# Kernel tuning notes

Hardware: AMD Instinct MI355X
Metric: run time of the kernel (lower is better)

## Reference

```python
import jax, jax.numpy as jnp
import numpy as np

N_NODES = 20000
N_EDGES = 200000
D_IN, D_H1, D_H2, D_OUT = 1433, 1000, 500, 7


def setup_inputs() -> dict:
    key = jax.random.key(0)
    ks = jax.random.split(key, 8)
    features = jax.random.normal(ks[0], (N_NODES, D_IN), dtype=jnp.float32)
    src = jax.random.randint(ks[1], (N_EDGES,), 0, N_NODES)
    dst = jax.random.randint(ks[2], (N_EDGES,), 0, N_NODES)
    W1 = jax.random.normal(ks[3], (D_IN, D_H1), dtype=jnp.float32) * 0.02
    b1 = jnp.zeros((D_H1,), dtype=jnp.float32)
    W2 = jax.random.normal(ks[4], (D_H1, D_H2), dtype=jnp.float32) * 0.02
    b2 = jnp.zeros((D_H2,), dtype=jnp.float32)
    W3 = jax.random.normal(ks[5], (D_H2, D_OUT), dtype=jnp.float32) * 0.02
    b3 = jnp.zeros((D_OUT,), dtype=jnp.float32)
    return {"features": features, "src": src, "dst": dst,
            "W1": W1, "b1": b1, "W2": W2, "b2": b2, "W3": W3, "b3": b3}


def reference(features, src, dst, W1, b1, W2, b2, W3, b3):
    N = features.shape[0]

    def agg(x):  # sum_tensors over incoming neighbors: h_i = sum_{(j->i) in E} x_j
        return jax.ops.segment_sum(x[src], dst, num_segments=N)

    # GCN layer 1: aggregate -> linear -> relu
    x = jax.nn.relu(agg(features) @ W1 + b1)       # [N, 1000]
    # GCN layer 2: aggregate -> linear -> relu (dropout = identity in eval)
    x = jax.nn.relu(agg(x) @ W2 + b2)              # [N, 500]
    # output linear -> relu (dropout = identity in eval)
    x = jax.nn.relu(x @ W3 + b3)                   # [N, 7]
    return x
```

## Files before the change

kernel.cpp:

```cpp
#include <hip/hip_runtime.h>
#include <hip/hip_bf16.h>


#define N_NODES 20000
#define N_EDGES 200000
#define D_IN    1433
#define D_H1    1000
#define D_H2    500
#define D_OUT   7

#define MPAD    20096
#define K1PAD   1440
#define N1PAD   1024
#define K2PAD   1024
#define N2PAD   512
#define H1STR   1008
#define H2STR   504
#define MBLK    157

typedef __attribute__((ext_vector_type(8))) short short8;
typedef __attribute__((ext_vector_type(8))) unsigned short ushort8_t;
typedef __attribute__((ext_vector_type(4))) float f32x4;

__device__ __forceinline__ unsigned short bf16_rne(float x) {
    unsigned int u = __float_as_uint(x);
    u = (u + 0x7FFFu + ((u >> 16) & 1u)) >> 16;
    return (unsigned short)u;
}
__device__ __forceinline__ float bf16_up(unsigned short h) {
    return __uint_as_float((unsigned int)h << 16);
}

__device__ __forceinline__ void gl_lds16(const unsigned short* g, unsigned short* lds) {
    __builtin_amdgcn_global_load_lds(
        (const __attribute__((address_space(1))) unsigned int*)g,
        (__attribute__((address_space(3))) unsigned int*)lds, 16, 0, 0);
}

__global__ __launch_bounds__(256) void count_deg(const int* __restrict__ dst,
                                                 int* __restrict__ offs) {
    int e = blockIdx.x * 256 + threadIdx.x;
    if (e < N_EDGES) atomicAdd(&offs[dst[e] + 1], 1);
}

__global__ __launch_bounds__(1024) void scan_csr(int* __restrict__ offs,
                                                 int* __restrict__ cursor, int n) {
    __shared__ int wsum[16];
    __shared__ int s_carry;
    const int t = threadIdx.x, lane = t & 63, wv = t >> 6;
    if (t == 0) s_carry = 0;
    __syncthreads();
    for (int base = 0; base < n; base += 1024) {
        int i = base + t;
        int v = (i < n) ? offs[i] : 0;
        #pragma unroll
        for (int s = 1; s < 64; s <<= 1) {
            int u = __shfl_up(v, s, 64);
            if (lane >= s) v += u;
        }
        if (lane == 63) wsum[wv] = v;
        __syncthreads();
        int prefix = s_carry;
        for (int k = 0; k < wv; ++k) prefix += wsum[k];
        v += prefix;
        if (i < n) {
            offs[i] = v;
            if (i < N_NODES) cursor[i] = v;
        }
        __syncthreads();
        if (t == 1023) s_carry = v;
    }
}

__global__ __launch_bounds__(256) void fill_csr(const int* __restrict__ src,
                                                const int* __restrict__ dst,
                                                int* __restrict__ cursor,
                                                int* __restrict__ srcs) {
    int e = blockIdx.x * 256 + threadIdx.x;
    if (e < N_EDGES) {
        int pos = atomicAdd(&cursor[dst[e]], 1);
        srcs[pos] = src[e];
    }
}

__global__ __launch_bounds__(256) void cast_features(const float* __restrict__ F,
                                                     unsigned int* __restrict__ out) {
    int row = blockIdx.x;
    int t = threadIdx.x;
    const float* fr = F + (size_t)row * D_IN;
    bool live = row < N_NODES;
    for (int kk = t; kk < K1PAD / 2; kk += 256) {
        int k0 = kk * 2;
        float a = (live && k0     < D_IN) ? fr[k0]     : 0.f;
        float b = (live && k0 + 1 < D_IN) ? fr[k0 + 1] : 0.f;
        out[(size_t)row * (K1PAD / 2) + kk] =
            (unsigned int)bf16_rne(a) | ((unsigned int)bf16_rne(b) << 16);
    }
}

template <int SR, int SC, int DR, int DC>
__global__ __launch_bounds__(256) void transpose_cast_pad(const float* __restrict__ src,
                                                          unsigned short* __restrict__ dst) {
    __shared__ float tile[32][33];
    int c0 = blockIdx.x * 32;
    int r0 = blockIdx.y * 32;
    int tx = threadIdx.x & 31, ty = threadIdx.x >> 5;
    #pragma unroll
    for (int p = 0; p < 4; ++p) {
        int r = r0 + ty + p * 8, c = c0 + tx;
        tile[ty + p * 8][tx] = (r < SR && c < SC) ? src[(size_t)r * SC + c] : 0.f;
    }
    __syncthreads();
    #pragma unroll
    for (int p = 0; p < 4; ++p) {
        int dr = c0 + ty + p * 8;
        int dc = r0 + tx;
        if (dr < DR && dc < DC) dst[(size_t)dr * DC + dc] = bf16_rne(tile[tx][ty + p * 8]);
    }
}

template <int KPAD, int NB>
__global__ __launch_bounds__(256) void gemm_mfma(const unsigned short* __restrict__ A,
                                                 const unsigned short* __restrict__ B,
                                                 unsigned short* __restrict__ C,
                                                 int M, int N, int OSTR) {
    __shared__ __align__(16) unsigned short sA[128 * 32];
    __shared__ __align__(16) unsigned short sB[128 * 32];
    const int bid = blockIdx.x;
    const int xcd = bid & 7;
    const int tt  = bid >> 3;
    const int nb  = tt % NB;
    const int mb  = (tt / NB) * 8 + xcd;
    if (mb >= MBLK) return;

    const int t = threadIdx.x;
    const int w = t >> 6, lane = t & 63;
    const int m0 = mb * 128, n0 = nb * 128;
    const int wm = (w >> 1) * 64, wn = (w & 1) * 64;

    const int srow = lane >> 2;
    const int skc  = ((lane & 3) ^ ((lane >> 3) & 3)) * 8;
    const int mrow = lane & 15, quad = lane >> 4;
    const int rslot = ((quad ^ ((mrow >> 1) & 3)) & 3) * 8;

    const unsigned short* Aptr = A + (size_t)(m0 + srow) * KPAD + skc;
    const unsigned short* Bptr = B + (size_t)(n0 + srow) * KPAD + skc;

    f32x4 acc[4][4] = {};

    for (int k0 = 0; k0 < KPAD; k0 += 32) {
        #pragma unroll
        for (int c = 0; c < 2; ++c) {
            int rbase = c * 64 + w * 16;
            gl_lds16(Aptr + (size_t)rbase * KPAD, &sA[rbase * 32]);
            gl_lds16(Bptr + (size_t)rbase * KPAD, &sB[rbase * 32]);
        }
        Aptr += 32; Bptr += 32;
        __syncthreads();

        short8 af[4], bf[4];
        #pragma unroll
        for (int mt = 0; mt < 4; ++mt)
            af[mt] = *(const short8*)&sA[(wm + mt * 16 + mrow) * 32 + rslot];
        #pragma unroll
        for (int nt = 0; nt < 4; ++nt)
            bf[nt] = *(const short8*)&sB[(wn + nt * 16 + mrow) * 32 + rslot];
        #pragma unroll
        for (int mt = 0; mt < 4; ++mt)
            #pragma unroll
            for (int nt = 0; nt < 4; ++nt)
                acc[mt][nt] = __builtin_amdgcn_mfma_f32_16x16x32_bf16(
                    af[mt], bf[nt], acc[mt][nt], 0, 0, 0);
        __syncthreads();
    }

    #pragma unroll
    for (int mt = 0; mt < 4; ++mt) {
        int m = m0 + wm + mt * 16 + quad * 4;
        #pragma unroll
        for (int nt = 0; nt < 4; ++nt) {
            int n = n0 + wn + nt * 16 + mrow;
            if (n >= N) continue;
            #pragma unroll
            for (int r = 0; r < 4; ++r)
                if (m + r < M) C[(size_t)(m + r) * OSTR + n] = bf16_rne(acc[mt][nt][r]);
        }
    }
}

__global__ __launch_bounds__(128) void agg1_bf16(const unsigned short* __restrict__ H,
                                                 const int* __restrict__ offs,
                                                 const int* __restrict__ srcs,
                                                 const float* __restrict__ bias,
                                                 unsigned short* __restrict__ X) {
    const int i = blockIdx.x, t = threadIdx.x;
    const bool active = t < 125;
    const int tc = active ? t : 124;
    ushort8_t o = (ushort8_t)0;
    if (i < N_NODES) {
        const int beg = offs[i], end = offs[i + 1];
        float s[8] = {};
        for (int e = beg; e < end; ++e) {
            const int j = srcs[e];
            ushort8_t v = *(const ushort8_t*)(H + (size_t)j * H1STR + tc * 8);
            #pragma unroll
            for (int u = 0; u < 8; ++u) s[u] += bf16_up(v[u]);
        }
        if (active) {
            #pragma unroll
            for (int u = 0; u < 8; ++u)
                o[u] = bf16_rne(fmaxf(s[u] + bias[t * 8 + u], 0.f));
        }
    }
    *(ushort8_t*)(X + (size_t)i * K2PAD + t * 8) = o;
}

__global__ __launch_bounds__(128) void agg2_out(const unsigned short* __restrict__ H,
                                                const int* __restrict__ offs,
                                                const int* __restrict__ srcs,
                                                const float* __restrict__ b2,
                                                const float* __restrict__ W3,
                                                const float* __restrict__ b3,
                                                float* __restrict__ out) {
    __shared__ float red[2][8];
    const int i = blockIdx.x, t = threadIdx.x;
    const bool active = t < 125;
    const int tc = active ? t : 124;
    const int beg = offs[i], end = offs[i + 1];
    float s[4] = {};
    for (int e = beg; e < end; ++e) {
        const int j = srcs[e];
        ushort4 v = *(const ushort4*)(H + (size_t)j * H2STR + tc * 4);
        s[0] += bf16_up(v.x); s[1] += bf16_up(v.y);
        s[2] += bf16_up(v.z); s[3] += bf16_up(v.w);
    }
    float acc[D_OUT] = {};
    if (active) {
        #pragma unroll
        for (int u = 0; u < 4; ++u) {
            float x = fmaxf(s[u] + b2[t * 4 + u], 0.f);
            const float* wr = W3 + (size_t)(t * 4 + u) * D_OUT;
            #pragma unroll
            for (int j = 0; j < D_OUT; ++j) acc[j] += x * wr[j];
        }
    }
    #pragma unroll
    for (int j = 0; j < D_OUT; ++j)
        #pragma unroll
        for (int off = 32; off; off >>= 1) acc[j] += __shfl_down(acc[j], off);
    const int lane = t & 63, wave = t >> 6;
    if (lane == 0) {
        #pragma unroll
        for (int j = 0; j < D_OUT; ++j) red[wave][j] = acc[j];
    }
    __syncthreads();
    if (t == 0) {
        #pragma unroll
        for (int j = 0; j < D_OUT; ++j)
            out[(size_t)i * D_OUT + j] = fmaxf(red[0][j] + red[1][j] + b3[j], 0.f);
    }
}

extern "C" void kernel_launch(void* const* d_in, const int* in_sizes, int n_in,
                              void* d_out, int out_size, void* d_ws, size_t ws_size,
                              hipStream_t stream) {
    const float* features = (const float*)d_in[0];
    const int*   src      = (const int*)d_in[1];
    const int*   dst      = (const int*)d_in[2];
    const float* W1       = (const float*)d_in[3];
    const float* b1       = (const float*)d_in[4];
    const float* W2       = (const float*)d_in[5];
    const float* b2       = (const float*)d_in[6];
    const float* W3       = (const float*)d_in[7];
    const float* b3       = (const float*)d_in[8];
    float* out = (float*)d_out;

    char* ws = (char*)d_ws;
    unsigned short* Fbf  = (unsigned short*)(ws + 0);
    unsigned short* X1bf = (unsigned short*)(ws + 0);
    unsigned short* H1   = (unsigned short*)(ws + 57876480);
    unsigned short* H2   = (unsigned short*)(ws + 57876480);
    unsigned short* W1T  = (unsigned short*)(ws + 98196480);
    unsigned short* W2T  = (unsigned short*)(ws + 101145600);
    int* offs   = (int*)(ws + 102194176);
    int* cursor = (int*)(ws + 102274304);
    int* srcs   = (int*)(ws + 102354432);

    hipMemsetAsync(offs, 0, (N_NODES + 1) * sizeof(int), stream);
    count_deg<<<(N_EDGES + 255) / 256, 256, 0, stream>>>(dst, offs);
    scan_csr<<<1, 1024, 0, stream>>>(offs, cursor, N_NODES + 1);
    fill_csr<<<(N_EDGES + 255) / 256, 256, 0, stream>>>(src, dst, cursor, srcs);

    cast_features<<<MPAD, 256, 0, stream>>>(features, (unsigned int*)Fbf);
    transpose_cast_pad<D_IN, D_H1, N1PAD, K1PAD>
        <<<dim3(N1PAD / 32, K1PAD / 32), 256, 0, stream>>>(W1, W1T);
    transpose_cast_pad<D_H1, D_H2, N2PAD, K2PAD>
        <<<dim3(N2PAD / 32, K2PAD / 32), 256, 0, stream>>>(W2, W2T);

    gemm_mfma<K1PAD, N1PAD / 128><<<8 * (N1PAD / 128) * 20, 256, 0, stream>>>(
        Fbf, W1T, H1, N_NODES, D_H1, H1STR);
    agg1_bf16<<<MPAD, 128, 0, stream>>>(H1, offs, srcs, b1, X1bf);

    gemm_mfma<K2PAD, N2PAD / 128><<<8 * (N2PAD / 128) * 20, 256, 0, stream>>>(
        X1bf, W2T, H2, N_NODES, D_H2, H2STR);
    agg2_out<<<N_NODES, 128, 0, stream>>>(H2, offs, srcs, b2, W3, b3, out);
}
```

Baseline: 457.5 us.

## Double GEMM K-tile to 64 with new LDS swizzle; unroll gather loops by four

The MFMA GEMM now stages 64-wide K slices into shared memory, using a new XOR swizzle, and runs two MFMA sub-steps per slice. This halves the number of barrier pairs per K loop. K1 is padded to 1472 so it divides by 64, and workspace offsets are shifted to match. Both aggregation kernels unroll the neighbor gather by four to keep more independent loads in flight. The larger padding adds a small amount of wasted work, and the doubled LDS footprint may lower occupancy.

New measurement: 439.3 us. 4.0% less time.

```diff
diff --git a/kernel.cpp b/kernel.cpp
--- a/kernel.cpp
+++ b/kernel.cpp
@@ -10,7 +10,7 @@
 #define D_OUT   7
 
 #define MPAD    20096
-#define K1PAD   1440
+#define K1PAD   1472
 #define N1PAD   1024
 #define K2PAD   1024
 #define N2PAD   512
@@ -124,8 +124,8 @@
                                                  const unsigned short* __restrict__ B,
                                                  unsigned short* __restrict__ C,
                                                  int M, int N, int OSTR) {
-    __shared__ __align__(16) unsigned short sA[128 * 32];
-    __shared__ __align__(16) unsigned short sB[128 * 32];
+    __shared__ __align__(16) unsigned short sA[128 * 64];
+    __shared__ __align__(16) unsigned short sB[128 * 64];
     const int bid = blockIdx.x;
     const int xcd = bid & 7;
     const int tt  = bid >> 3;
@@ -138,39 +138,45 @@
     const int m0 = mb * 128, n0 = nb * 128;
     const int wm = (w >> 1) * 64, wn = (w & 1) * 64;
 
-    const int srow = lane >> 2;
-    const int skc  = ((lane & 3) ^ ((lane >> 3) & 3)) * 8;
+    const int srowo = lane >> 3;
+    const int skc   = ((lane & 7) ^ srowo) * 8;
     const int mrow = lane & 15, quad = lane >> 4;
-    const int rslot = ((quad ^ ((mrow >> 1) & 3)) & 3) * 8;
-
-    const unsigned short* Aptr = A + (size_t)(m0 + srow) * KPAD + skc;
-    const unsigned short* Bptr = B + (size_t)(n0 + srow) * KPAD + skc;
+
+    const unsigned short* Aptr = A + (size_t)(m0 + srowo) * KPAD + skc;
+    const unsigned short* Bptr = B + (size_t)(n0 + srowo) * KPAD + skc;
 
     f32x4 acc[4][4] = {};
 
-    for (int k0 = 0; k0 < KPAD; k0 += 32) {
-        #pragma unroll
-        for (int c = 0; c < 2; ++c) {
-            int rbase = c * 64 + w * 16;
-            gl_lds16(Aptr + (size_t)rbase * KPAD, &sA[rbase * 32]);
-            gl_lds16(Bptr + (size_t)rbase * KPAD, &sB[rbase * 32]);
-        }
-        Aptr += 32; Bptr += 32;
+    for (int k0 = 0; k0 < KPAD; k0 += 64) {
+        #pragma unroll
+        for (int c = 0; c < 4; ++c) {
+            const int rbase = c * 32 + w * 8;
+            gl_lds16(Aptr + (size_t)rbase * KPAD, &sA[rbase * 64]);
+            gl_lds16(Bptr + (size_t)rbase * KPAD, &sB[rbase * 64]);
+        }
+        Aptr += 64; Bptr += 64;
         __syncthreads();
 
-        short8 af[4], bf[4];
-        #pragma unroll
-        for (int mt = 0; mt < 4; ++mt)
-            af[mt] = *(const short8*)&sA[(wm + mt * 16 + mrow) * 32 + rslot];
-        #pragma unroll
-        for (int nt = 0; nt < 4; ++nt)
-            bf[nt] = *(const short8*)&sB[(wn + nt * 16 + mrow) * 32 + rslot];
-        #pragma unroll
-        for (int mt = 0; mt < 4; ++mt)
-            #pragma unroll
-            for (int nt = 0; nt < 4; ++nt)
-                acc[mt][nt] = __builtin_amdgcn_mfma_f32_16x16x32_bf16(
-                    af[mt], bf[nt], acc[mt][nt], 0, 0, 0);
+        #pragma unroll
+        for (int s = 0; s < 2; ++s) {
+            short8 af[4], bf[4];
+            #pragma unroll
+            for (int mt = 0; mt < 4; ++mt) {
+                int r = wm + mt * 16 + mrow;
+                af[mt] = *(const short8*)&sA[r * 64 + (((s * 4 + quad) ^ (mrow & 7)) * 8)];
+            }
+            #pragma unroll
+            for (int nt = 0; nt < 4; ++nt) {
+                int r = wn + nt * 16 + mrow;
+                bf[nt] = *(const short8*)&sB[r * 64 + (((s * 4 + quad) ^ (mrow & 7)) * 8)];
+            }
+            #pragma unroll
+            for (int mt = 0; mt < 4; ++mt)
+                #pragma unroll
+                for (int nt = 0; nt < 4; ++nt)
+                    acc[mt][nt] = __builtin_amdgcn_mfma_f32_16x16x32_bf16(
+                        af[mt], bf[nt], acc[mt][nt], 0, 0, 0);
+        }
         __syncthreads();
     }
 
@@ -199,10 +205,22 @@
     ushort8_t o = (ushort8_t)0;
     if (i < N_NODES) {
         const int beg = offs[i], end = offs[i + 1];
+        const unsigned short* Hc = H + tc * 8;
         float s[8] = {};
-        for (int e = beg; e < end; ++e) {
-            const int j = srcs[e];
-            ushort8_t v = *(const ushort8_t*)(H + (size_t)j * H1STR + tc * 8);
+        int e = beg;
+        for (; e + 4 <= end; e += 4) {
+            int j0 = srcs[e], j1 = srcs[e + 1], j2 = srcs[e + 2], j3 = srcs[e + 3];
+            ushort8_t v0 = *(const ushort8_t*)(Hc + (size_t)j0 * H1STR);
+            ushort8_t v1 = *(const ushort8_t*)(Hc + (size_t)j1 * H1STR);
+            ushort8_t v2 = *(const ushort8_t*)(Hc + (size_t)j2 * H1STR);
+            ushort8_t v3 = *(const ushort8_t*)(Hc + (size_t)j3 * H1STR);
+            #pragma unroll
+            for (int u = 0; u < 8; ++u)
+                s[u] += (bf16_up(v0[u]) + bf16_up(v1[u])) +
+                        (bf16_up(v2[u]) + bf16_up(v3[u]));
+        }
+        for (; e < end; ++e) {
+            ushort8_t v = *(const ushort8_t*)(Hc + (size_t)srcs[e] * H1STR);
             #pragma unroll
             for (int u = 0; u < 8; ++u) s[u] += bf16_up(v[u]);
         }
@@ -227,10 +245,22 @@
     const bool active = t < 125;
     const int tc = active ? t : 124;
     const int beg = offs[i], end = offs[i + 1];
+    const unsigned short* Hc = H + tc * 4;
     float s[4] = {};
-    for (int e = beg; e < end; ++e) {
-        const int j = srcs[e];
-        ushort4 v = *(const ushort4*)(H + (size_t)j * H2STR + tc * 4);
+    int e = beg;
+    for (; e + 4 <= end; e += 4) {
+        int j0 = srcs[e], j1 = srcs[e + 1], j2 = srcs[e + 2], j3 = srcs[e + 3];
+        ushort4 v0 = *(const ushort4*)(Hc + (size_t)j0 * H2STR);
+        ushort4 v1 = *(const ushort4*)(Hc + (size_t)j1 * H2STR);
+        ushort4 v2 = *(const ushort4*)(Hc + (size_t)j2 * H2STR);
+        ushort4 v3 = *(const ushort4*)(Hc + (size_t)j3 * H2STR);
+        s[0] += (bf16_up(v0.x) + bf16_up(v1.x)) + (bf16_up(v2.x) + bf16_up(v3.x));
+        s[1] += (bf16_up(v0.y) + bf16_up(v1.y)) + (bf16_up(v2.y) + bf16_up(v3.y));
+        s[2] += (bf16_up(v0.z) + bf16_up(v1.z)) + (bf16_up(v2.z) + bf16_up(v3.z));
+        s[3] += (bf16_up(v0.w) + bf16_up(v1.w)) + (bf16_up(v2.w) + bf16_up(v3.w));
+    }
+    for (; e < end; ++e) {
+        ushort4 v = *(const ushort4*)(Hc + (size_t)srcs[e] * H2STR);
         s[0] += bf16_up(v.x); s[1] += bf16_up(v.y);
         s[2] += bf16_up(v.z); s[3] += bf16_up(v.w);
     }
@@ -278,13 +308,13 @@
     char* ws = (char*)d_ws;
     unsigned short* Fbf  = (unsigned short*)(ws + 0);
     unsigned short* X1bf = (unsigned short*)(ws + 0);
-    unsigned short* H1   = (unsigned short*)(ws + 57876480);
-    unsigned short* H2   = (unsigned short*)(ws + 57876480);
-    unsigned short* W1T  = (unsigned short*)(ws + 98196480);
-    unsigned short* W2T  = (unsigned short*)(ws + 101145600);
-    int* offs   = (int*)(ws + 102194176);
-    int* cursor = (int*)(ws + 102274304);
-    int* srcs   = (int*)(ws + 102354432);
+    unsigned short* H1   = (unsigned short*)(ws + 59162624);
+    unsigned short* H2   = (unsigned short*)(ws + 59162624);
+    unsigned short* W1T  = (unsigned short*)(ws + 99482624);
+    unsigned short* W2T  = (unsigned short*)(ws + 102497280);
+    int* offs   = (int*)(ws + 103545856);
+    int* cursor = (int*)(ws + 103625984);
+    int* srcs   = (int*)(ws + 103706112);
 
     hipMemsetAsync(offs, 0, (N_NODES + 1) * sizeof(int), stream);
     count_deg<<<(N_EDGES + 255) / 256, 256, 0, stream>>>(dst, offs);
```
